# Optimization experiments

Hardware: AMD Instinct MI355X
Metric: run time of the kernel (lower is better)

Reference implementation:

```python
import jax, jax.numpy as jnp
import numpy as np

CODE_NUM = 12288
GRAPH = 128      # graph_size: embedding width / GRU input
HIDDEN = 128     # GRU hidden = t_output_size = time_size (required by scatter/broadcast)
ATT = 64         # t_attention_size


def setup_inputs() -> dict:
    key = jax.random.key(0)
    ks = jax.random.split(key, 20)
    s = 0.05
    # disjoint 3-way membership masks (m1/m2/m3), some codes in no set
    cat = jax.random.randint(ks[0], (CODE_NUM,), 0, 4)
    divided = jax.nn.one_hot(cat, 4, dtype=jnp.int32)[:, :3]
    return {
        "interval": jnp.asarray(3.5, jnp.float32),
        "co_embeddings": jax.random.normal(ks[1], (CODE_NUM, GRAPH), jnp.float32),
        "no_embeddings": jax.random.normal(ks[2], (CODE_NUM, GRAPH), jnp.float32),
        "unrelated_embeddings": jax.random.normal(ks[3], (CODE_NUM, GRAPH), jnp.float32),
        "hidden_state": jax.random.normal(ks[4], (CODE_NUM, HIDDEN), jnp.float32),
        "divided": divided,
        # GRUCell params (torch layout: [3H, in], gates r|z|n)
        "W_ih": jax.random.normal(ks[5], (3 * HIDDEN, GRAPH), jnp.float32) * s,
        "W_hh": jax.random.normal(ks[6], (3 * HIDDEN, HIDDEN), jnp.float32) * s,
        "b_ih": jax.random.normal(ks[7], (3 * HIDDEN,), jnp.float32) * s,
        "b_hh": jax.random.normal(ks[8], (3 * HIDDEN,), jnp.float32) * s,
        # SingleHeadAttentionLayer params
        "Wq": jax.random.normal(ks[9], (ATT, GRAPH), jnp.float32) * s,
        "bq": jax.random.normal(ks[10], (ATT,), jnp.float32) * s,
        "Wk": jax.random.normal(ks[11], (ATT, GRAPH), jnp.float32) * s,
        "bk": jax.random.normal(ks[12], (ATT,), jnp.float32) * s,
        "Wv": jax.random.normal(ks[13], (HIDDEN, GRAPH), jnp.float32) * s,
        "bv": jax.random.normal(ks[14], (HIDDEN,), jnp.float32) * s,
        # time_layer: Linear(1, time_size)
        "Wt": jax.random.normal(ks[15], (HIDDEN, 1), jnp.float32) * s,
        "bt": jax.random.normal(ks[16], (HIDDEN,), jnp.float32) * s,
        "t": 1,
        "is_last": 0,
    }


def _gru_cell(x, h, W_ih, W_hh, b_ih, b_hh):
    gi = x @ W_ih.T + b_ih          # [N, 3H]
    gh = h @ W_hh.T + b_hh          # [N, 3H]
    i_r, i_z, i_n = jnp.split(gi, 3, axis=-1)
    h_r, h_z, h_n = jnp.split(gh, 3, axis=-1)
    r = jax.nn.sigmoid(i_r + h_r)
    z = jax.nn.sigmoid(i_z + h_z)
    n = jnp.tanh(i_n + r * h_n)
    return (1.0 - z) * n + z * h


def reference(interval, co_embeddings, no_embeddings, unrelated_embeddings,
              hidden_state, divided, W_ih, W_hh, b_ih, b_hh,
              Wq, bq, Wk, bk, Wv, bv, Wt, bt, t, is_last):
    dt = co_embeddings.dtype
    # time feature: tanh(Linear(1/log(interval + e)))
    x_t = 1.0 / jnp.log(interval + jnp.e)                       # scalar
    time_features = jnp.tanh(x_t * Wt[:, 0] + bt)               # [H]

    if is_last:
        out = _gru_cell(co_embeddings, hidden_state, W_ih, W_hh, b_ih, b_hh)
        return (out + time_features, None)

    m1 = divided[:, 0] > 0
    m2 = divided[:, 1] > 0
    m3 = divided[:, 2] > 0
    m23 = m2 | m3
    NEG = jnp.finfo(dt).min

    # --- m1 branch: GRUCell is row-wise, so compute on all rows and mask ---
    h_gru = _gru_cell(co_embeddings, hidden_state, W_ih, W_hh, b_ih, b_hh)  # [N, H]
    output_m1 = jnp.max(jnp.where(m1[:, None], h_gru, NEG), axis=0)        # [H]

    # --- m2/m3 branch: attention over the m23 subset (mask-based, order-free)
    # query rows: m2 -> no_embeddings, m3 -> unrelated_embeddings
    q_full = jnp.where(m2[:, None], no_embeddings, unrelated_embeddings)   # [N, G]
    Q = q_full @ Wq.T + bq                                                 # [N, A]
    K = co_embeddings @ Wk.T + bk                                          # [N, A]
    V = co_embeddings @ Wv.T + bv                                          # [N, H]
    scores = (Q @ K.T) / jnp.sqrt(jnp.asarray(ATT, dt))                    # [N, N]
    scores = jnp.where(m23[None, :], scores, NEG)                          # keys restricted to m23
    attn = jax.nn.softmax(scores, axis=-1)
    h_att = jnp.tanh(attn @ V)                                             # [N, H]
    output_m23 = jnp.max(jnp.where(m23[:, None], h_att, NEG), axis=0)      # [H]

    # scatter: m2/m3 rows written after m1 rows (m23 takes precedence)
    h_new = jnp.where(m23[:, None], h_att,
                      jnp.where(m1[:, None], h_gru, jnp.zeros((), dt)))

    output = jnp.maximum(output_m1, output_m23)
    return (output + time_features, h_new)
```

## Files before the change

### kernel.cpp

```cpp
#include <hip/hip_runtime.h>
#include <hip/hip_bf16.h>
#include <math.h>

#define N_CODES 12288
#define G 128
#define H 128
#define ATT 64
#define NEGF (-3.4028234663852886e38f)
#define NSEG 8
#define QT 64
#define QMAX 7168
#define NQTA (QMAX / QT)

typedef __attribute__((ext_vector_type(8))) short bf16x8;
typedef __attribute__((ext_vector_type(4))) float f32x4;
typedef __hip_bfloat16 bf16;
#define MFMA16(a, b, c) __builtin_amdgcn_mfma_f32_16x16x32_bf16(a, b, c, 0, 0, 0)

struct __align__(16) Ws {
  int n1;
  int n23;
  int cnt;
  int pad_;
  int idx1[N_CODES];
  int rows23[N_CODES];
  int flags23[N_CODES];
  unsigned maxu[128];
  float tf[128];
  float lseg[NSEG * QMAX];
  float bqkv[256];
  float b2[512];
  bf16 Wqkv[16 * 4 * 64 * 8];
  bf16 W2[32 * 8 * 64 * 8];
  bf16 Qb[(size_t)N_CODES * ATT];
  bf16 Kf[(size_t)N_CODES * ATT];
  bf16 Vf[(size_t)N_CODES * H];
  bf16 Oseg[(size_t)NSEG * QMAX * H];
};

__device__ inline uint2 pack4(float4 v) {
  union { bf16 b[4]; uint2 u; } cv;
  cv.b[0] = __float2bfloat16(v.x);
  cv.b[1] = __float2bfloat16(v.y);
  cv.b[2] = __float2bfloat16(v.z);
  cv.b[3] = __float2bfloat16(v.w);
  return cv.u;
}

__device__ inline float bf2f(short s) {
  union { unsigned u; float f; } c;
  c.u = ((unsigned)(unsigned short)s) << 16;
  return c.f;
}

__device__ inline unsigned fkey(float f) {
  unsigned b = __float_as_uint(f);
  return (b & 0x80000000u) ? ~b : (b | 0x80000000u);
}
__device__ inline float funkey(unsigned u) {
  unsigned b = (u & 0x80000000u) ? (u & 0x7fffffffu) : ~u;
  return __uint_as_float(b);
}

__global__ void k_setup(const int* __restrict__ divided,
                        const float* __restrict__ Wq, const float* __restrict__ bq,
                        const float* __restrict__ Wk, const float* __restrict__ bk,
                        const float* __restrict__ Wv, const float* __restrict__ bv,
                        const float* __restrict__ W_ih, const float* __restrict__ W_hh,
                        const float* __restrict__ b_ih, const float* __restrict__ b_hh,
                        const float* __restrict__ interval, const float* __restrict__ Wt,
                        const float* __restrict__ bt, Ws* ws) {
  int bid = blockIdx.x;
  int t = threadIdx.x;
  if (bid < 48) {
    int r = bid * 256 + t;
    int m1 = divided[r * 3 + 0] > 0;
    int m2 = divided[r * 3 + 1] > 0;
    int m3 = divided[r * 3 + 2] > 0;
    if (m1) {
      int p = atomicAdd(&ws->n1, 1);
      ws->idx1[p] = r;
    }
    if (m2 | m3) {
      int p = atomicAdd(&ws->n23, 1);
      ws->rows23[p] = r;
      ws->flags23[p] = m2;
    }
    return;
  }
  if (bid < 80) {
    int idx = (bid - 48) * 256 + t;
    int c = idx >> 5, k = (idx & 31) * 4;
    float4 v;
    if (c < 64) {
      v = *(const float4*)&Wq[c * G + k];
      v.x *= 0.125f; v.y *= 0.125f; v.z *= 0.125f; v.w *= 0.125f;
    } else if (c < 128) {
      v = *(const float4*)&Wk[(c - 64) * G + k];
    } else {
      v = *(const float4*)&Wv[(c - 128) * G + k];
    }
    int NB = c >> 4, lo = c & 15, ks = k >> 5, hi = (k >> 3) & 3, j = k & 7;
    *(uint2*)&ws->Wqkv[((NB * 4 + ks) * 64 + hi * 16 + lo) * 8 + j] = pack4(v);
    return;
  }
  if (bid < 208) {
    int idx = (bid - 80) * 256 + t;
    int c = idx >> 6, k = (idx & 63) * 4;
    int g = c >> 7, d = c & 127;
    float4 v = {0.f, 0.f, 0.f, 0.f};
    if (g == 0) v = (k < 128) ? *(const float4*)&W_ih[d * G + k]
                              : *(const float4*)&W_hh[d * H + (k - 128)];
    else if (g == 1) v = (k < 128) ? *(const float4*)&W_ih[(128 + d) * G + k]
                                   : *(const float4*)&W_hh[(128 + d) * H + (k - 128)];
    else if (g == 2) { if (k < 128) v = *(const float4*)&W_ih[(256 + d) * G + k]; }
    else { if (k >= 128) v = *(const float4*)&W_hh[(256 + d) * H + (k - 128)]; }
    int NB = c >> 4, lo = c & 15, ks = k >> 5, hi = (k >> 3) & 3, j = k & 7;
    *(uint2*)&ws->W2[((NB * 8 + ks) * 64 + hi * 16 + lo) * 8 + j] = pack4(v);
    return;
  }
  if (t < 128) {
    float xt = 1.0f / logf(interval[0] + 2.718281828459045f);
    ws->tf[t] = tanhf(xt * Wt[t] + bt[t]);
    ws->maxu[t] = 0u;
  }
  for (int i = t; i < 768; i += 256) {
    if (i < 256) {
      float v;
      if (i < 64) v = bq[i] * 0.125f;
      else if (i < 128) v = bk[i - 64];
      else v = bv[i - 128];
      ws->bqkv[i] = v;
    } else {
      int c = i - 256;
      int g = c >> 7, d = c & 127;
      float v;
      if (g == 0) v = b_ih[d] + b_hh[d];
      else if (g == 1) v = b_ih[128 + d] + b_hh[128 + d];
      else if (g == 2) v = b_ih[256 + d];
      else v = b_hh[256 + d];
      ws->b2[c] = v;
    }
  }
}

__launch_bounds__(256)
__global__ void k_mm(const float* __restrict__ co, const float* __restrict__ no_e,
                     const float* __restrict__ un_e, const float* __restrict__ hs,
                     Ws* ws, float* __restrict__ h_new) {
  __shared__ __align__(16) bf16 sm[8704];
  int bid = blockIdx.x;
  int t = threadIdx.x;
  int w = t >> 6, lane = t & 63, lo = lane & 15, hi = lane >> 4;

  if (bid < 448) {
    int n23 = ws->n23;
    int q0 = bid * 16;
    if (q0 >= n23) return;
    bf16(*Aq)[136] = (bf16(*)[136])sm;
    bf16(*Ac)[136] = (bf16(*)[136])(sm + 2176);
    for (int it = 0; it < 2; ++it) {
      int idx = it * 256 + t;
      int rr = idx >> 5, c4 = idx & 31;
      uint2 pq = {0, 0}, pc = {0, 0};
      int p = q0 + rr;
      if (p < n23) {
        int row = ws->rows23[p];
        const float* srcq = ws->flags23[p] ? no_e : un_e;
        pq = pack4(*(const float4*)&srcq[(size_t)row * G + c4 * 4]);
        pc = pack4(*(const float4*)&co[(size_t)row * G + c4 * 4]);
      }
      *(uint2*)&Aq[rr][c4 * 4] = pq;
      *(uint2*)&Ac[rr][c4 * 4] = pc;
    }
    __syncthreads();
    const bf16(*At)[136] = (w == 0) ? Aq : Ac;
    f32x4 acc[4];
#pragma unroll
    for (int nb = 0; nb < 4; ++nb) acc[nb] = (f32x4){0.f, 0.f, 0.f, 0.f};
#pragma unroll
    for (int ks = 0; ks < 4; ++ks) {
      bf16x8 af = *(const bf16x8*)&At[lo][ks * 32 + hi * 8];
#pragma unroll
      for (int nb = 0; nb < 4; ++nb) {
        bf16x8 bfr = *(const bf16x8*)&ws->Wqkv[(((w * 4 + nb) * 4 + ks) * 64 + lane) * 8];
        acc[nb] = MFMA16(af, bfr, acc[nb]);
      }
    }
#pragma unroll
    for (int nb = 0; nb < 4; ++nb) {
      int c = w * 64 + nb * 16 + lo;
      float bias = ws->bqkv[c];
#pragma unroll
      for (int r = 0; r < 4; ++r) {
        int p = q0 + hi * 4 + r;
        if (p >= n23) continue;
        bf16 bv16 = __float2bfloat16(acc[nb][r] + bias);
        if (c < 64) {
          ws->Qb[(size_t)p * ATT + c] = bv16;
        } else if (c < 128) {
          int d = c - 64;
          ws->Kf[(((p >> 4) * 2 + (d >> 5)) * 64 + ((d >> 3) & 3) * 16 + (p & 15)) * 8 + (d & 7)] = bv16;
        } else {
          int d = c - 128;
          ws->Vf[((((p >> 6) * 8 + (d >> 4)) * 2 + ((p >> 5) & 1)) * 64 + ((p >> 3) & 3) * 16 + (d & 15)) * 8 + (p & 7)] = bv16;
        }
      }
    }
  } else {
    int n1 = ws->n1;
    int q0 = (bid - 448) * 16;
    if (q0 >= n1) return;
    bf16(*A2)[264] = (bf16(*)[264])sm;
    for (int it = 0; it < 4; ++it) {
      int idx = it * 256 + t;
      int rr = idx >> 6, c4 = idx & 63;
      uint2 pk = {0, 0};
      int p = q0 + rr;
      if (p < n1) {
        int row = ws->idx1[p];
        float4 v = (c4 < 32) ? *(const float4*)&co[(size_t)row * G + c4 * 4]
                             : *(const float4*)&hs[(size_t)row * H + (c4 - 32) * 4];
        pk = pack4(v);
      }
      *(uint2*)&A2[rr][c4 * 4] = pk;
    }
    __syncthreads();
    f32x4 acc[8];
#pragma unroll
    for (int x = 0; x < 8; ++x) acc[x] = (f32x4){0.f, 0.f, 0.f, 0.f};
#pragma unroll
    for (int ks = 0; ks < 8; ++ks) {
      bf16x8 af = *(const bf16x8*)&A2[lo][ks * 32 + hi * 8];
#pragma unroll
      for (int g = 0; g < 4; ++g) {
#pragma unroll
        for (int nb2 = 0; nb2 < 2; ++nb2) {
          int NB = g * 8 + w * 2 + nb2;
          bf16x8 bfr = *(const bf16x8*)&ws->W2[((NB * 8 + ks) * 64 + lane) * 8];
          acc[g * 2 + nb2] = MFMA16(af, bfr, acc[g * 2 + nb2]);
        }
      }
    }
    float mx2[2] = {NEGF, NEGF};
#pragma unroll
    for (int nb2 = 0; nb2 < 2; ++nb2) {
      int d = w * 32 + nb2 * 16 + lo;
      float br = ws->b2[d], bz = ws->b2[128 + d], bin_ = ws->b2[256 + d], bhn = ws->b2[384 + d];
#pragma unroll
      for (int r = 0; r < 4; ++r) {
        int p = q0 + hi * 4 + r;
        if (p >= n1) continue;
        int row = ws->idx1[p];
        float rs = acc[0 + nb2][r] + br;
        float zs = acc[2 + nb2][r] + bz;
        float in_ = acc[4 + nb2][r] + bin_;
        float hn = acc[6 + nb2][r] + bhn;
        float rg = 1.f / (1.f + __expf(-rs));
        float zg = 1.f / (1.f + __expf(-zs));
        float ng = tanhf(in_ + rg * hn);
        float h0 = hs[(size_t)row * H + d];
        float hv = (1.f - zg) * ng + zg * h0;
        h_new[(size_t)row * H + d] = hv;
        mx2[nb2] = fmaxf(mx2[nb2], hv);
      }
    }
#pragma unroll
    for (int nb2 = 0; nb2 < 2; ++nb2) {
      float m = mx2[nb2];
      m = fmaxf(m, __shfl_xor(m, 16));
      m = fmaxf(m, __shfl_xor(m, 32));
      if (hi == 0) atomicMax(&ws->maxu[w * 32 + nb2 * 16 + lo], fkey(m));
    }
  }
}

__launch_bounds__(256)
__global__ void k_attn(const Ws* __restrict__ ws, Ws* __restrict__ wso) {
  int n23 = ws->n23;
  int bid = blockIdx.x;
  int q0 = (bid % NQTA) * QT;
  int seg = bid / NQTA;
  if (q0 >= n23) return;
  int segk = (((n23 + NSEG - 1) / NSEG) + 63) & ~63;
  int s0 = seg * segk;
  int t = threadIdx.x;
  if (s0 >= n23) {
    for (int idx = t; idx < QT * 32; idx += 256) {
      int q = q0 + (idx >> 5);
      if (q < n23) {
        uint2 z2 = {0, 0};
        *(uint2*)&wso->Oseg[((size_t)seg * QMAX + q) * H + (idx & 31) * 4] = z2;
      }
    }
    if (t < QT && q0 + t < n23) wso->lseg[seg * QMAX + q0 + t] = 0.f;
    return;
  }
  int send = min(s0 + segk, n23);

  int w = t >> 6, lane = t & 63, lo = lane & 15, hi = lane >> 4;

  __shared__ bf16 Pl[64][72];
  __shared__ float Lw[4][64];

  bf16x8 qf[4][2];
#pragma unroll
  for (int qsub = 0; qsub < 4; ++qsub)
#pragma unroll
    for (int s = 0; s < 2; ++s)
      qf[qsub][s] =
          *(const bf16x8*)&ws->Qb[(size_t)(q0 + qsub * 16 + lo) * ATT + s * 32 + hi * 8];

  f32x4 acc[2][4];
#pragma unroll
  for (int ddl = 0; ddl < 2; ++ddl)
#pragma unroll
    for (int qsub = 0; qsub < 4; ++qsub) acc[ddl][qsub] = (f32x4){0.f, 0.f, 0.f, 0.f};
  float lacc[4] = {0.f, 0.f, 0.f, 0.f};

  for (int c0 = s0; c0 < send; c0 += 64) {
    int kb = (c0 >> 4) + w;
    bf16x8 kf0 = *(const bf16x8*)&ws->Kf[((size_t)(kb * 2 + 0) * 64 + lane) * 8];
    bf16x8 kf1 = *(const bf16x8*)&ws->Kf[((size_t)(kb * 2 + 1) * 64 + lane) * 8];
#pragma unroll
    for (int qsub = 0; qsub < 4; ++qsub) {
      f32x4 s_ = {0.f, 0.f, 0.f, 0.f};
      s_ = MFMA16(kf0, qf[qsub][0], s_);
      s_ = MFMA16(kf1, qf[qsub][1], s_);
      union { bf16 b[4]; uint2 u; } tu;
      float sl = 0.f;
#pragma unroll
      for (int r = 0; r < 4; ++r) {
        int key = c0 + w * 16 + hi * 4 + r;
        float p = (key < send) ? __expf(s_[r]) : 0.f;
        sl += p;
        tu.b[r] = __float2bfloat16(p);
      }
      *(uint2*)&Pl[qsub * 16 + lo][w * 16 + hi * 4] = tu.u;
      sl += __shfl_xor(sl, 16);
      sl += __shfl_xor(sl, 32);
      lacc[qsub] += sl;
    }
    __syncthreads();

    int kc = c0 >> 6;
#pragma unroll
    for (int s = 0; s < 2; ++s) {
      bf16x8 pf[4];
#pragma unroll
      for (int qsub = 0; qsub < 4; ++qsub)
        pf[qsub] = *(const bf16x8*)&Pl[qsub * 16 + lo][s * 32 + hi * 8];
#pragma unroll
      for (int ddl = 0; ddl < 2; ++ddl) {
        bf16x8 vf =
            *(const bf16x8*)&ws->Vf[((size_t)(kc * 16 + (w * 2 + ddl) * 2 + s) * 64 + lane) * 8];
#pragma unroll
        for (int qsub = 0; qsub < 4; ++qsub) acc[ddl][qsub] = MFMA16(vf, pf[qsub], acc[ddl][qsub]);
      }
    }
    __syncthreads();
  }

  if (hi == 0) {
#pragma unroll
    for (int qsub = 0; qsub < 4; ++qsub) Lw[w][qsub * 16 + lo] = lacc[qsub];
  }
  __syncthreads();
  if (t < QT) {
    int q = q0 + t;
    if (q < n23) wso->lseg[seg * QMAX + q] = Lw[0][t] + Lw[1][t] + Lw[2][t] + Lw[3][t];
  }
#pragma unroll
  for (int qsub = 0; qsub < 4; ++qsub) {
    int q = q0 + qsub * 16 + lo;
    if (q < n23) {
#pragma unroll
      for (int ddl = 0; ddl < 2; ++ddl) {
        union { bf16 b[4]; uint2 u; } tmp;
#pragma unroll
        for (int r = 0; r < 4; ++r) tmp.b[r] = __float2bfloat16(acc[ddl][qsub][r]);
        *(uint2*)&wso->Oseg[((size_t)seg * QMAX + q) * H + w * 32 + ddl * 16 + hi * 4] = tmp.u;
      }
    }
  }
}

__global__ void k_merge(const Ws* __restrict__ ws, float* __restrict__ h_new, Ws* wso,
                        float* __restrict__ out) {
  int n23 = ws->n23;
  int qb = blockIdx.x * 32;
  if (qb >= n23) return;
  int t = threadIdx.x;
  int d = t & 127, half = t >> 7;
  float mx = NEGF;
  for (int qi = 0; qi < 16; ++qi) {
    int q = qb + half * 16 + qi;
    if (q >= n23) break;
    float o = 0.f, L = 0.f;
#pragma unroll
    for (int s = 0; s < NSEG; ++s) {
      o += bf2f(((const short*)ws->Oseg)[((size_t)s * QMAX + q) * H + d]);
      L += ws->lseg[s * QMAX + q];
    }
    float h = tanhf(o / L);
    h_new[(size_t)ws->rows23[q] * H + d] = h;
    mx = fmaxf(mx, h);
  }
  __shared__ float red[256];
  __shared__ int lastv;
  red[t] = mx;
  __syncthreads();
  if (t < 128) atomicMax(&wso->maxu[t], fkey(fmaxf(red[t], red[t + 128])));
  __syncthreads();
  if (t == 0) {
    __threadfence();
    int nact = (n23 + 31) >> 5;
    lastv = (atomicAdd(&wso->cnt, 1) == nact - 1) ? 1 : 0;
  }
  __syncthreads();
  if (lastv && t < 128) {
    unsigned u = atomicOr(&wso->maxu[t], 0u);
    out[t] = funkey(u) + ws->tf[t];
  }
}

extern "C" void kernel_launch(void* const* d_in, const int* in_sizes, int n_in,
                              void* d_out, int out_size, void* d_ws, size_t ws_size,
                              hipStream_t stream) {
  const float* interval = (const float*)d_in[0];
  const float* co = (const float*)d_in[1];
  const float* no_e = (const float*)d_in[2];
  const float* un_e = (const float*)d_in[3];
  const float* hs = (const float*)d_in[4];
  const int* divided = (const int*)d_in[5];
  const float* W_ih = (const float*)d_in[6];
  const float* W_hh = (const float*)d_in[7];
  const float* b_ih = (const float*)d_in[8];
  const float* b_hh = (const float*)d_in[9];
  const float* Wq = (const float*)d_in[10];
  const float* bq = (const float*)d_in[11];
  const float* Wk = (const float*)d_in[12];
  const float* bk = (const float*)d_in[13];
  const float* Wv = (const float*)d_in[14];
  const float* bv = (const float*)d_in[15];
  const float* Wt = (const float*)d_in[16];
  const float* bt = (const float*)d_in[17];

  float* out = (float*)d_out;
  float* h_new = out + 128;
  Ws* ws = (Ws*)d_ws;

  hipMemsetAsync(d_out, 0, (size_t)out_size * sizeof(float), stream);
  hipMemsetAsync(ws, 0, 16, stream);

  k_setup<<<209, 256, 0, stream>>>(divided, Wq, bq, Wk, bk, Wv, bv, W_ih, W_hh, b_ih, b_hh,
                                   interval, Wt, bt, ws);
  k_mm<<<704, 256, 0, stream>>>(co, no_e, un_e, hs, ws, h_new);
  k_attn<<<NQTA * NSEG, 256, 0, stream>>>(ws, ws);
  k_merge<<<QMAX / 32, 256, 0, stream>>>(ws, h_new, ws, out);
}
```

Baseline: 190.2 us.

## Prefetch K/V fragments in attention, double key segments, drop full output memset

The attention loop now loads the next K fragments while the current scores are exponentiated. It also hoists all V fragment loads ahead of the PV MFMAs to hide global-load latency. The key-split count doubles and the kernel gets a minimum-occupancy launch bound to improve parallelism across CUs, at the cost of more partial results for the merge kernel. The full memset of the output buffer is replaced by zeroing only rows that belong to no mask inside the setup kernel, which saves a large memory write.

```diff
diff --git a/kernel.cpp b/kernel.cpp
--- a/kernel.cpp
+++ b/kernel.cpp
@@ -7,7 +7,7 @@
 #define H 128
 #define ATT 64
 #define NEGF (-3.4028234663852886e38f)
-#define NSEG 8
+#define NSEG 16
 #define QT 64
 #define QMAX 7168
 #define NQTA (QMAX / QT)
@@ -69,7 +69,7 @@
                         const float* __restrict__ W_ih, const float* __restrict__ W_hh,
                         const float* __restrict__ b_ih, const float* __restrict__ b_hh,
                         const float* __restrict__ interval, const float* __restrict__ Wt,
-                        const float* __restrict__ bt, Ws* ws) {
+                        const float* __restrict__ bt, Ws* ws, float* __restrict__ h_new) {
   int bid = blockIdx.x;
   int t = threadIdx.x;
   if (bid < 48) {
@@ -85,6 +85,12 @@
       int p = atomicAdd(&ws->n23, 1);
       ws->rows23[p] = r;
       ws->flags23[p] = m2;
+    }
+    if (!(m1 | m2 | m3)) {
+      float4 z = {0.f, 0.f, 0.f, 0.f};
+      float4* hr = (float4*)&h_new[(size_t)r * H];
+#pragma unroll
+      for (int i = 0; i < 32; ++i) hr[i] = z;
     }
     return;
   }
@@ -275,7 +281,7 @@
   }
 }
 
-__launch_bounds__(256)
+__launch_bounds__(256, 4)
 __global__ void k_attn(const Ws* __restrict__ ws, Ws* __restrict__ wso) {
   int n23 = ws->n23;
   int bid = blockIdx.x;
@@ -318,21 +324,31 @@
     for (int qsub = 0; qsub < 4; ++qsub) acc[ddl][qsub] = (f32x4){0.f, 0.f, 0.f, 0.f};
   float lacc[4] = {0.f, 0.f, 0.f, 0.f};
 
+  int kb0 = (s0 >> 4) + w;
+  bf16x8 kfA0 = *(const bf16x8*)&ws->Kf[((size_t)(kb0 * 2 + 0) * 64 + lane) * 8];
+  bf16x8 kfA1 = *(const bf16x8*)&ws->Kf[((size_t)(kb0 * 2 + 1) * 64 + lane) * 8];
+
   for (int c0 = s0; c0 < send; c0 += 64) {
-    int kb = (c0 >> 4) + w;
-    bf16x8 kf0 = *(const bf16x8*)&ws->Kf[((size_t)(kb * 2 + 0) * 64 + lane) * 8];
-    bf16x8 kf1 = *(const bf16x8*)&ws->Kf[((size_t)(kb * 2 + 1) * 64 + lane) * 8];
+    int cn = (c0 + 64 < send) ? (c0 + 64) : c0;
+    f32x4 sa[4];
 #pragma unroll
     for (int qsub = 0; qsub < 4; ++qsub) {
       f32x4 s_ = {0.f, 0.f, 0.f, 0.f};
-      s_ = MFMA16(kf0, qf[qsub][0], s_);
-      s_ = MFMA16(kf1, qf[qsub][1], s_);
+      s_ = MFMA16(kfA0, qf[qsub][0], s_);
+      s_ = MFMA16(kfA1, qf[qsub][1], s_);
+      sa[qsub] = s_;
+    }
+    int kbn = (cn >> 4) + w;
+    bf16x8 kfB0 = *(const bf16x8*)&ws->Kf[((size_t)(kbn * 2 + 0) * 64 + lane) * 8];
+    bf16x8 kfB1 = *(const bf16x8*)&ws->Kf[((size_t)(kbn * 2 + 1) * 64 + lane) * 8];
+#pragma unroll
+    for (int qsub = 0; qsub < 4; ++qsub) {
       union { bf16 b[4]; uint2 u; } tu;
       float sl = 0.f;
 #pragma unroll
       for (int r = 0; r < 4; ++r) {
         int key = c0 + w * 16 + hi * 4 + r;
-        float p = (key < send) ? __expf(s_[r]) : 0.f;
+        float p = (key < send) ? __expf(sa[qsub][r]) : 0.f;
         sl += p;
         tu.b[r] = __float2bfloat16(p);
       }
@@ -344,6 +360,13 @@
     __syncthreads();
 
     int kc = c0 >> 6;
+    bf16x8 vf[2][2];
+#pragma unroll
+    for (int s = 0; s < 2; ++s)
+#pragma unroll
+      for (int ddl = 0; ddl < 2; ++ddl)
+        vf[s][ddl] =
+            *(const bf16x8*)&ws->Vf[((size_t)(kc * 16 + (w * 2 + ddl) * 2 + s) * 64 + lane) * 8];
 #pragma unroll
     for (int s = 0; s < 2; ++s) {
       bf16x8 pf[4];
@@ -351,14 +374,14 @@
       for (int qsub = 0; qsub < 4; ++qsub)
         pf[qsub] = *(const bf16x8*)&Pl[qsub * 16 + lo][s * 32 + hi * 8];
 #pragma unroll
-      for (int ddl = 0; ddl < 2; ++ddl) {
-        bf16x8 vf =
-            *(const bf16x8*)&ws->Vf[((size_t)(kc * 16 + (w * 2 + ddl) * 2 + s) * 64 + lane) * 8];
-#pragma unroll
-        for (int qsub = 0; qsub < 4; ++qsub) acc[ddl][qsub] = MFMA16(vf, pf[qsub], acc[ddl][qsub]);
-      }
+      for (int ddl = 0; ddl < 2; ++ddl)
+#pragma unroll
+        for (int qsub = 0; qsub < 4; ++qsub)
+          acc[ddl][qsub] = MFMA16(vf[s][ddl], pf[qsub], acc[ddl][qsub]);
     }
     __syncthreads();
+    kfA0 = kfB0;
+    kfA1 = kfB1;
   }
 
   if (hi == 0) {
@@ -450,11 +473,10 @@
   float* h_new = out + 128;
   Ws* ws = (Ws*)d_ws;
 
-  hipMemsetAsync(d_out, 0, (size_t)out_size * sizeof(float), stream);
   hipMemsetAsync(ws, 0, 16, stream);
 
   k_setup<<<209, 256, 0, stream>>>(divided, Wq, bq, Wk, bk, Wv, bv, W_ih, W_hh, b_ih, b_hh,
-                                   interval, Wt, bt, ws);
+                                   interval, Wt, bt, ws, h_new);
   k_mm<<<704, 256, 0, stream>>>(co, no_e, un_e, hs, ws, h_new);
   k_attn<<<NQTA * NSEG, 256, 0, stream>>>(ws, ws);
   k_merge<<<QMAX / 32, 256, 0, stream>>>(ws, h_new, ws, out);
```

Measured after the change: 196.4 us. 1.03x slower.

## Drop output memset, zero unassigned rows in setup, vectorize merge, hoist V loads

Applied to the files above, without the earlier changes.

Removes the full-output hipMemsetAsync. Rows that belong to no mask set are now zeroed directly inside k_setup, and the first 128 output entries are written by the final merge block. k_merge is rewritten so each thread handles 8 contiguous dims of one query with bf16x8 vector loads and float4 stores, and a 16-query shared max reduction replaces the old scalar loop. In k_attn, the V fragment loads for the PV MFMAs are hoisted ahead of the loop so they can overlap. The cost is more registers in k_attn, and correctness now relies on out[0..127] always being written by the last merge block.

```diff
diff --git a/kernel.cpp b/kernel.cpp
--- a/kernel.cpp
+++ b/kernel.cpp
@@ -69,7 +69,7 @@
                         const float* __restrict__ W_ih, const float* __restrict__ W_hh,
                         const float* __restrict__ b_ih, const float* __restrict__ b_hh,
                         const float* __restrict__ interval, const float* __restrict__ Wt,
-                        const float* __restrict__ bt, Ws* ws) {
+                        const float* __restrict__ bt, Ws* ws, float* __restrict__ h_new) {
   int bid = blockIdx.x;
   int t = threadIdx.x;
   if (bid < 48) {
@@ -85,6 +85,12 @@
       int p = atomicAdd(&ws->n23, 1);
       ws->rows23[p] = r;
       ws->flags23[p] = m2;
+    }
+    if (!(m1 | m2 | m3)) {
+      float4 z = {0.f, 0.f, 0.f, 0.f};
+      float4* hr = (float4*)&h_new[(size_t)r * H];
+#pragma unroll
+      for (int i = 0; i < 32; ++i) hr[i] = z;
     }
     return;
   }
@@ -344,6 +350,13 @@
     __syncthreads();
 
     int kc = c0 >> 6;
+    bf16x8 vf[2][2];
+#pragma unroll
+    for (int s = 0; s < 2; ++s)
+#pragma unroll
+      for (int ddl = 0; ddl < 2; ++ddl)
+        vf[s][ddl] =
+            *(const bf16x8*)&ws->Vf[((size_t)(kc * 16 + (w * 2 + ddl) * 2 + s) * 64 + lane) * 8];
 #pragma unroll
     for (int s = 0; s < 2; ++s) {
       bf16x8 pf[4];
@@ -351,12 +364,10 @@
       for (int qsub = 0; qsub < 4; ++qsub)
         pf[qsub] = *(const bf16x8*)&Pl[qsub * 16 + lo][s * 32 + hi * 8];
 #pragma unroll
-      for (int ddl = 0; ddl < 2; ++ddl) {
-        bf16x8 vf =
-            *(const bf16x8*)&ws->Vf[((size_t)(kc * 16 + (w * 2 + ddl) * 2 + s) * 64 + lane) * 8];
-#pragma unroll
-        for (int qsub = 0; qsub < 4; ++qsub) acc[ddl][qsub] = MFMA16(vf, pf[qsub], acc[ddl][qsub]);
-      }
+      for (int ddl = 0; ddl < 2; ++ddl)
+#pragma unroll
+        for (int qsub = 0; qsub < 4; ++qsub)
+          acc[ddl][qsub] = MFMA16(vf[s][ddl], pf[qsub], acc[ddl][qsub]);
     }
     __syncthreads();
   }
@@ -388,33 +399,54 @@
 __global__ void k_merge(const Ws* __restrict__ ws, float* __restrict__ h_new, Ws* wso,
                         float* __restrict__ out) {
   int n23 = ws->n23;
-  int qb = blockIdx.x * 32;
+  int qb = blockIdx.x * 16;
   if (qb >= n23) return;
   int t = threadIdx.x;
-  int d = t & 127, half = t >> 7;
-  float mx = NEGF;
-  for (int qi = 0; qi < 16; ++qi) {
-    int q = qb + half * 16 + qi;
-    if (q >= n23) break;
-    float o = 0.f, L = 0.f;
+  int ql = t >> 4, d8 = (t & 15) * 8;
+  int q = qb + ql;
+
+  __shared__ float red[16][128];
+  float h8[8];
+  bool act = q < n23;
+  if (act) {
+    float o[8];
+#pragma unroll
+    for (int j = 0; j < 8; ++j) o[j] = 0.f;
+    float L = 0.f;
 #pragma unroll
     for (int s = 0; s < NSEG; ++s) {
-      o += bf2f(((const short*)ws->Oseg)[((size_t)s * QMAX + q) * H + d]);
+      bf16x8 ov = *(const bf16x8*)&ws->Oseg[((size_t)s * QMAX + q) * H + d8];
+#pragma unroll
+      for (int j = 0; j < 8; ++j) o[j] += bf2f(ov[j]);
       L += ws->lseg[s * QMAX + q];
     }
-    float h = tanhf(o / L);
-    h_new[(size_t)ws->rows23[q] * H + d] = h;
-    mx = fmaxf(mx, h);
-  }
-  __shared__ float red[256];
+    float linv = 1.0f / L;
+    float4 h0, h1;
+#pragma unroll
+    for (int j = 0; j < 8; ++j) h8[j] = tanhf(o[j] * linv);
+    h0.x = h8[0]; h0.y = h8[1]; h0.z = h8[2]; h0.w = h8[3];
+    h1.x = h8[4]; h1.y = h8[5]; h1.z = h8[6]; h1.w = h8[7];
+    float* hr = &h_new[(size_t)ws->rows23[q] * H + d8];
+    *(float4*)hr = h0;
+    *(float4*)(hr + 4) = h1;
+  } else {
+#pragma unroll
+    for (int j = 0; j < 8; ++j) h8[j] = NEGF;
+  }
+#pragma unroll
+  for (int j = 0; j < 8; ++j) red[ql][d8 + j] = h8[j];
+  __syncthreads();
+  if (t < 128) {
+    float m = NEGF;
+#pragma unroll
+    for (int ql2 = 0; ql2 < 16; ++ql2) m = fmaxf(m, red[ql2][t]);
+    atomicMax(&wso->maxu[t], fkey(m));
+  }
   __shared__ int lastv;
-  red[t] = mx;
-  __syncthreads();
-  if (t < 128) atomicMax(&wso->maxu[t], fkey(fmaxf(red[t], red[t + 128])));
   __syncthreads();
   if (t == 0) {
     __threadfence();
-    int nact = (n23 + 31) >> 5;
+    int nact = (n23 + 15) >> 4;
     lastv = (atomicAdd(&wso->cnt, 1) == nact - 1) ? 1 : 0;
   }
   __syncthreads();
@@ -450,12 +482,11 @@
   float* h_new = out + 128;
   Ws* ws = (Ws*)d_ws;
 
-  hipMemsetAsync(d_out, 0, (size_t)out_size * sizeof(float), stream);
   hipMemsetAsync(ws, 0, 16, stream);
 
   k_setup<<<209, 256, 0, stream>>>(divided, Wq, bq, Wk, bk, Wv, bv, W_ih, W_hh, b_ih, b_hh,
-                                   interval, Wt, bt, ws);
+                                   interval, Wt, bt, ws, h_new);
   k_mm<<<704, 256, 0, stream>>>(co, no_e, un_e, hs, ws, h_new);
   k_attn<<<NQTA * NSEG, 256, 0, stream>>>(ws, ws);
-  k_merge<<<QMAX / 32, 256, 0, stream>>>(ws, h_new, ws, out);
-}
+  k_merge<<<(QMAX + 15) / 16, 256, 0, stream>>>(ws, h_new, ws, out);
+}
```

New measurement: 182.8 us. 3.9% less time.
